# Kernel tuning notes

Measured on AMD Instinct MI355X. Metric: run time of the kernel, lower is better.

The kernel has to match this reference:

```python
import jax, jax.numpy as jnp
import numpy as np

T_RES, X_RES, Y_RES, LEVEL_DIM = 600, 300, 300, 2
N_POINTS = 2_000_000
STD = 1e-4


def setup_inputs() -> dict:
    key = jax.random.key(0)
    k_in, k_emb = jax.random.split(key)
    inputs = jax.random.uniform(k_in, (N_POINTS, 3), dtype=jnp.float32)
    embeddings = jax.random.uniform(
        k_emb, (T_RES, X_RES, Y_RES, LEVEL_DIM), dtype=jnp.float32,
        minval=-STD, maxval=STD)
    return {"inputs": inputs, "embeddings": embeddings}


def reference(inputs, embeddings):
    t_res, x_res, y_res, _ = embeddings.shape
    # round-to-nearest index per axis, clamped to valid range
    t_idx = jnp.clip(((t_res - 1) * inputs[:, 0] + 0.5).astype(jnp.int64), 0, t_res - 1)
    x_idx = jnp.clip(((x_res - 1) * inputs[:, 1] + 0.5).astype(jnp.int64), 0, x_res - 1)
    y_idx = jnp.clip(((y_res - 1) * inputs[:, 2] + 0.5).astype(jnp.int64), 0, y_res - 1)
    offs = jnp.array([-1, 0, 1], dtype=jnp.int64)
    vx = jnp.clip(x_idx[:, None] + offs, 0, x_res - 1)  # [N,3]
    vy = jnp.clip(y_idx[:, None] + offs, 0, y_res - 1)  # [N,3]
    # gather all 9 neighbors at once: [N,3,3,D]; (i,j) row-major matches the
    # original nested for i / for j concat order
    feats = embeddings[t_idx[:, None, None], vx[:, :, None], vy[:, None, :], :]
    n = feats.shape[0]
    return feats.reshape(n, 9 * embeddings.shape[-1])
```

## Files before the change

### kernel.cpp

```cpp
#include <hip/hip_runtime.h>


#define T_RES 600
#define X_RES 300
#define Y_RES 300
#define BLK 256

__global__ __launch_bounds__(BLK) void sparsegrid_gather(
    const float* __restrict__ inputs,
    const float* __restrict__ emb,
    float* __restrict__ out,
    int n)
{
    __shared__ float lds[BLK * 19];

    int tid  = threadIdx.x;
    int base = blockIdx.x * BLK;
    int i    = base + tid;
    int npts = n - base;
    if (npts > BLK) npts = BLK;

    if (tid < npts) {
        float t = inputs[3 * i + 0];
        float x = inputs[3 * i + 1];
        float y = inputs[3 * i + 2];

        int ti = (int)__fadd_rn(__fmul_rn((float)(T_RES - 1), t), 0.5f);
        int xi = (int)__fadd_rn(__fmul_rn((float)(X_RES - 1), x), 0.5f);
        int yi = (int)__fadd_rn(__fmul_rn((float)(Y_RES - 1), y), 0.5f);
        ti = min(max(ti, 0), T_RES - 1);
        xi = min(max(xi, 0), X_RES - 1);
        yi = min(max(yi, 0), Y_RES - 1);

        int xs0 = max(xi - 1, 0), xs2 = min(xi + 1, X_RES - 1);
        int ys0 = max(yi - 1, 0), ys1 = yi, ys2 = min(yi + 1, Y_RES - 1);

        const float2* __restrict__ e2 = (const float2*)emb;
        int tb = ti * X_RES;
        int r0 = (tb + xs0) * Y_RES;
        int r1 = (tb + xi ) * Y_RES;
        int r2 = (tb + xs2) * Y_RES;

        float2 v0 = e2[r0 + ys0];
        float2 v1 = e2[r0 + ys1];
        float2 v2 = e2[r0 + ys2];
        float2 v3 = e2[r1 + ys0];
        float2 v4 = e2[r1 + ys1];
        float2 v5 = e2[r1 + ys2];
        float2 v6 = e2[r2 + ys0];
        float2 v7 = e2[r2 + ys1];
        float2 v8 = e2[r2 + ys2];

        float* row = &lds[tid * 19];
        row[0]  = v0.x; row[1]  = v0.y;
        row[2]  = v1.x; row[3]  = v1.y;
        row[4]  = v2.x; row[5]  = v2.y;
        row[6]  = v3.x; row[7]  = v3.y;
        row[8]  = v4.x; row[9]  = v4.y;
        row[10] = v5.x; row[11] = v5.y;
        row[12] = v6.x; row[13] = v6.y;
        row[14] = v7.x; row[15] = v7.y;
        row[16] = v8.x; row[17] = v8.y;
    }

    __syncthreads();

    int total2 = npts * 9;
    float2* oblk = (float2*)(out + (size_t)base * 18);
    #pragma unroll
    for (int k = 0; k < 9; ++k) {
        int d2 = tid + BLK * k;
        if (d2 < total2) {
            int p = d2 / 9;
            int e = d2 - p * 9;
            float2 w;
            w.x = lds[p * 19 + 2 * e];
            w.y = lds[p * 19 + 2 * e + 1];
            oblk[d2] = w;
        }
    }
}

extern "C" void kernel_launch(void* const* d_in, const int* in_sizes, int n_in,
                              void* d_out, int out_size, void* d_ws, size_t ws_size,
                              hipStream_t stream) {
    const float* inputs = (const float*)d_in[0];
    const float* emb    = (const float*)d_in[1];
    float* out          = (float*)d_out;

    int n = in_sizes[0] / 3;
    int grid = (n + BLK - 1) / BLK;
    sparsegrid_gather<<<grid, BLK, 0, stream>>>(inputs, emb, out, n);
}
```

Measured before the change: 155.3 us.

## Use row-wise vector gathers, nontemporal I/O and 16-byte output stores

Each of the three neighbour rows is now read with one 16-byte load plus one 8-byte load from a clamped base, and a set of selects handles the border cases. This replaces nine separate 8-byte gathers. Inputs are read and outputs written with nontemporal hints. Full blocks write the output in 16-byte stores instead of 8-byte ones. The cost is extra select logic and per-element divides when repacking from LDS.

Measured after the change: 192.2 us. 23.8% more time.

```diff
diff --git a/kernel.cpp b/kernel.cpp
--- a/kernel.cpp
+++ b/kernel.cpp
@@ -5,6 +5,10 @@
 #define X_RES 300
 #define Y_RES 300
 #define BLK 256
+
+typedef float f4a8 __attribute__((ext_vector_type(4), aligned(8)));
+typedef float f4   __attribute__((ext_vector_type(4)));
+typedef float f2   __attribute__((ext_vector_type(2)));
 
 __global__ __launch_bounds__(BLK) void sparsegrid_gather(
     const float* __restrict__ inputs,
@@ -21,9 +25,9 @@
     if (npts > BLK) npts = BLK;
 
     if (tid < npts) {
-        float t = inputs[3 * i + 0];
-        float x = inputs[3 * i + 1];
-        float y = inputs[3 * i + 2];
+        float t = __builtin_nontemporal_load(inputs + 3 * i + 0);
+        float x = __builtin_nontemporal_load(inputs + 3 * i + 1);
+        float y = __builtin_nontemporal_load(inputs + 3 * i + 2);
 
         int ti = (int)__fadd_rn(__fmul_rn((float)(T_RES - 1), t), 0.5f);
         int xi = (int)__fadd_rn(__fmul_rn((float)(X_RES - 1), x), 0.5f);
@@ -32,51 +36,80 @@
         xi = min(max(xi, 0), X_RES - 1);
         yi = min(max(yi, 0), Y_RES - 1);
 
-        int xs0 = max(xi - 1, 0), xs2 = min(xi + 1, X_RES - 1);
-        int ys0 = max(yi - 1, 0), ys1 = yi, ys2 = min(yi + 1, Y_RES - 1);
+        int xb = min(max(xi - 1, 0), X_RES - 3);
+        int yb = min(max(yi - 1, 0), Y_RES - 3);
+        bool x0 = (xi == 0), x2 = (xi == X_RES - 1);
+        bool y0 = (yi == 0), y2 = (yi == Y_RES - 1);
 
-        const float2* __restrict__ e2 = (const float2*)emb;
-        int tb = ti * X_RES;
-        int r0 = (tb + xs0) * Y_RES;
-        int r1 = (tb + xi ) * Y_RES;
-        int r2 = (tb + xs2) * Y_RES;
+        const f2* __restrict__ e2 = (const f2*)emb;
+        int RA = (ti * X_RES + xb) * Y_RES + yb;
+        int RB = RA + Y_RES;
+        int RC = RB + Y_RES;
 
-        float2 v0 = e2[r0 + ys0];
-        float2 v1 = e2[r0 + ys1];
-        float2 v2 = e2[r0 + ys2];
-        float2 v3 = e2[r1 + ys0];
-        float2 v4 = e2[r1 + ys1];
-        float2 v5 = e2[r1 + ys2];
-        float2 v6 = e2[r2 + ys0];
-        float2 v7 = e2[r2 + ys1];
-        float2 v8 = e2[r2 + ys2];
+        f4a8 a01 = *(const f4a8*)(e2 + RA);  f2 a2 = e2[RA + 2];
+        f4a8 b01 = *(const f4a8*)(e2 + RB);  f2 b2 = e2[RB + 2];
+        f4a8 c01 = *(const f4a8*)(e2 + RC);  f2 c2 = e2[RC + 2];
+
+        f2 aS0 = {a01.x, a01.y}, aS1 = {a01.z, a01.w};
+        f2 bS0 = {b01.x, b01.y}, bS1 = {b01.z, b01.w};
+        f2 cS0 = {c01.x, c01.y}, cS1 = {c01.z, c01.w};
+
+        f2 a0 = y2 ? aS1 : aS0, a1v = y0 ? aS0 : (y2 ? a2 : aS1), a2v = y0 ? aS1 : a2;
+        f2 b0 = y2 ? bS1 : bS0, b1v = y0 ? bS0 : (y2 ? b2 : bS1), b2v = y0 ? bS1 : b2;
+        f2 c0 = y2 ? cS1 : cS0, c1v = y0 ? cS0 : (y2 ? c2 : cS1), c2v = y0 ? cS1 : c2;
+
+        f2 r0_0 = x2 ? b0  : a0,  r0_1 = x2 ? b1v : a1v, r0_2 = x2 ? b2v : a2v;
+        f2 r1_0 = x0 ? a0  : (x2 ? c0  : b0 );
+        f2 r1_1 = x0 ? a1v : (x2 ? c1v : b1v);
+        f2 r1_2 = x0 ? a2v : (x2 ? c2v : b2v);
+        f2 r2_0 = x0 ? b0  : c0,  r2_1 = x0 ? b1v : c1v, r2_2 = x0 ? b2v : c2v;
 
         float* row = &lds[tid * 19];
-        row[0]  = v0.x; row[1]  = v0.y;
-        row[2]  = v1.x; row[3]  = v1.y;
-        row[4]  = v2.x; row[5]  = v2.y;
-        row[6]  = v3.x; row[7]  = v3.y;
-        row[8]  = v4.x; row[9]  = v4.y;
-        row[10] = v5.x; row[11] = v5.y;
-        row[12] = v6.x; row[13] = v6.y;
-        row[14] = v7.x; row[15] = v7.y;
-        row[16] = v8.x; row[17] = v8.y;
+        row[0]  = r0_0.x; row[1]  = r0_0.y;
+        row[2]  = r0_1.x; row[3]  = r0_1.y;
+        row[4]  = r0_2.x; row[5]  = r0_2.y;
+        row[6]  = r1_0.x; row[7]  = r1_0.y;
+        row[8]  = r1_1.x; row[9]  = r1_1.y;
+        row[10] = r1_2.x; row[11] = r1_2.y;
+        row[12] = r2_0.x; row[13] = r2_0.y;
+        row[14] = r2_1.x; row[15] = r2_1.y;
+        row[16] = r2_2.x; row[17] = r2_2.y;
     }
 
     __syncthreads();
 
-    int total2 = npts * 9;
-    float2* oblk = (float2*)(out + (size_t)base * 18);
-    #pragma unroll
-    for (int k = 0; k < 9; ++k) {
-        int d2 = tid + BLK * k;
-        if (d2 < total2) {
-            int p = d2 / 9;
-            int e = d2 - p * 9;
-            float2 w;
-            w.x = lds[p * 19 + 2 * e];
-            w.y = lds[p * 19 + 2 * e + 1];
-            oblk[d2] = w;
+    if (npts == BLK) {
+        f4* oblk4 = (f4*)(out + (size_t)base * 18);
+        #pragma unroll
+        for (int k = 0; k < 5; ++k) {
+            int q = tid + BLK * k;
+            if (q < (BLK * 18) / 4) {
+                unsigned idx = 4u * q;
+                f4 w;
+                #pragma unroll
+                for (int c = 0; c < 4; ++c) {
+                    unsigned id = idx + c;
+                    unsigned p = id / 18u;
+                    unsigned e = id - 18u * p;
+                    w[c] = lds[p * 19 + e];
+                }
+                __builtin_nontemporal_store(w, oblk4 + q);
+            }
+        }
+    } else {
+        int total2 = npts * 9;
+        f2* oblk = (f2*)(out + (size_t)base * 18);
+        #pragma unroll
+        for (int k = 0; k < 9; ++k) {
+            int d2 = tid + BLK * k;
+            if (d2 < total2) {
+                int p = d2 / 9;
+                int e = d2 - p * 9;
+                f2 w;
+                w.x = lds[p * 19 + 2 * e];
+                w.y = lds[p * 19 + 2 * e + 1];
+                __builtin_nontemporal_store(w, oblk + d2);
+            }
         }
     }
 }
```
